# Kernel tuning notes

Measured on AMD Instinct MI355X. Metric: run time of the kernel, lower is better.

Reference implementation:

```python
import jax, jax.numpy as jnp
import numpy as np

N = 8192   # number of nodes / relationships
D = 64     # input_dim == output_dim


def setup_inputs() -> dict:
    key = jax.random.key(0)
    ks = jax.random.split(key, 13)
    s = 0.05
    return {
        "object_features": jax.random.normal(ks[0], (N, D), dtype=jnp.float32),
        "relationship_features": jax.random.normal(ks[1], (N, D), dtype=jnp.float32),
        # sparse-ish 0/1 adjacency, as in the reference usage
        "adjacency_matrix": (jax.random.uniform(ks[2], (N, N)) < 0.05).astype(jnp.float32),
        # nn.Linear params, stored as [in, out] (i.e. torch weight transposed)
        "W_obj": jax.random.normal(ks[3], (D, D), dtype=jnp.float32) * s,
        "b_obj": jax.random.normal(ks[4], (D,), dtype=jnp.float32) * s,
        "W_nobj": jax.random.normal(ks[5], (D, D), dtype=jnp.float32) * s,
        "b_nobj": jax.random.normal(ks[6], (D,), dtype=jnp.float32) * s,
        "W_rel": jax.random.normal(ks[7], (D, D), dtype=jnp.float32) * s,
        "b_rel": jax.random.normal(ks[8], (D,), dtype=jnp.float32) * s,
        "W_skip": jax.random.normal(ks[9], (D, D), dtype=jnp.float32) * s,
        "b_skip": jax.random.normal(ks[10], (D,), dtype=jnp.float32) * s,
        "Wa_w": jax.random.normal(ks[11], (2 * D, 1), dtype=jnp.float32) * s,  # Linear(2D -> 1)
        "Wa_b": jax.random.normal(ks[12], (1,), dtype=jnp.float32) * s,
    }


def reference(object_features, relationship_features, adjacency_matrix,
              W_obj, b_obj, W_nobj, b_nobj, W_rel, b_rel,
              W_skip, b_skip, Wa_w, Wa_b):
    x, r, A = object_features, relationship_features, adjacency_matrix
    d = x.shape[1]

    # message projections (small GEMMs)
    msgs_obj = x @ W_obj + b_obj                      # [N, D]
    msgs_nbr = A.T @ (x @ W_nobj + b_nobj)            # [N, D]
    msgs_rel = r @ W_rel + b_rel                      # [N, D]
    aggregated = msgs_obj + msgs_nbr + msgs_rel       # [N, D]

    # Wa(concat([x_i, r_j])) = x_i @ Wa_w[:d] + r_j @ Wa_w[d:] + Wa_b
    # (avoids materializing the [N, N, 2D] concat the torch code builds)
    sx = x @ Wa_w[:d]                                 # [N, 1] (per row i)
    sr = r @ Wa_w[d:]                                 # [N, 1] (per col j)
    scores = (sx + sr.T + Wa_b) * A                   # [N, N], masked-by-multiply
    attention = jax.nn.softmax(scores, axis=1)        # [N, N]

    # sum_j attn[i, j] * aggregated[i, :]  (exactly the torch broadcast-sum over dim=1)
    attn_agg = jnp.einsum('ij,ik->ik', attention, aggregated)  # [N, D]

    return x @ W_skip + b_skip + attn_agg
```

## Files before the change

kernel.cpp:

```cpp
#include <hip/hip_runtime.h>

typedef __attribute__((ext_vector_type(8))) short short8;
typedef __attribute__((ext_vector_type(4))) float f32x4;

#define NN 8192
#define DD 64

__device__ inline unsigned short f2bf(float f){
  unsigned b = __float_as_uint(f);
  b = (b + 0x7fffu + ((b >> 16) & 1u)) >> 16;
  return (unsigned short)b;
}


__global__ __launch_bounds__(256) void k_proj(
    const float* __restrict__ x, const float* __restrict__ r,
    const float* __restrict__ Wobj,  const float* __restrict__ bobj,
    const float* __restrict__ Wnobj, const float* __restrict__ bnobj,
    const float* __restrict__ Wrel,  const float* __restrict__ brel,
    const float* __restrict__ Wskip, const float* __restrict__ bskip,
    float* __restrict__ accT, unsigned short* __restrict__ yT)
{
  const int i  = blockIdx.x * 256 + threadIdx.x;
  const int d0 = blockIdx.y * 4;

  float ay[4] = {0.f,0.f,0.f,0.f}, az[4] = {0.f,0.f,0.f,0.f};
  const float4* xp = (const float4*)(x + (size_t)i * DD);
  const float4* rp = (const float4*)(r + (size_t)i * DD);

#pragma unroll
  for (int kb = 0; kb < 4; kb++){
    float xv[16], rv[16];
#pragma unroll
    for (int p = 0; p < 4; p++){
      float4 u = xp[kb*4 + p];
      xv[4*p+0]=u.x; xv[4*p+1]=u.y; xv[4*p+2]=u.z; xv[4*p+3]=u.w;
      float4 v = rp[kb*4 + p];
      rv[4*p+0]=v.x; rv[4*p+1]=v.y; rv[4*p+2]=v.z; rv[4*p+3]=v.w;
    }
#pragma unroll
    for (int kk = 0; kk < 16; kk++){
      const int wb = (kb*16 + kk) * DD + d0;
      const float xk = xv[kk], rk = rv[kk];
#pragma unroll
      for (int t = 0; t < 4; t++){
        ay[t] += xk * Wnobj[wb + t];
        az[t] += xk * Wobj [wb + t];
        az[t] += xk * Wskip[wb + t];
        az[t] += rk * Wrel [wb + t];
      }
    }
  }

#pragma unroll
  for (int t = 0; t < 4; t++){
    ay[t] += bnobj[d0 + t];
    az[t] += bobj[d0 + t] + brel[d0 + t] + bskip[d0 + t];
    yT[(size_t)(d0 + t) * NN + i]   = f2bf(ay[t]);
    accT[(size_t)(d0 + t) * NN + i] = az[t];
  }
}

#define BN 128
#define KSPLIT 8
#define KCH (NN / KSPLIT)
#define NIT (KCH / 64)
#define ASZ (64 * 128)
#define YSZ (64 * 72)

__global__ __launch_bounds__(256) void k_spmm(
    const float* __restrict__ A,
    const unsigned short* __restrict__ yT,
    float* __restrict__ part)
{
  __shared__ short Alds[2 * ASZ];
  __shared__ short Ylds[2 * YSZ];

  const int tid  = threadIdx.x;
  const int lane = tid & 63;
  const int wave = tid >> 6;
  const int q    = lane >> 4;
  const int nn   = lane & 15;

  const int j0     = blockIdx.x * BN;
  const int kstart = blockIdx.y * KCH;

  const int c4 = tid & 31;
  const int kr = tid >> 5;
  const int cY = tid & 7;
  const int m0 = tid >> 3;

  const float* ap          = A  + (size_t)(kstart + kr) * NN + j0 + c4 * 4;
  const unsigned short* yp = yT + (size_t)m0 * NN + kstart + cY * 8;

  uint4 abuf[8], ybuf[2];
  auto gload = [&](){
#pragma unroll
    for (int p = 0; p < 8; p++)
      abuf[p] = *(const uint4*)(ap + (size_t)p * 8 * NN);
#pragma unroll
    for (int p = 0; p < 2; p++)
      ybuf[p] = *(const uint4*)(yp + (size_t)p * 32 * NN);
    ap += 64 * NN;
    yp += 64;
  };
  auto stage = [&](int buf){
    short* Ab = &Alds[buf * ASZ];
    short* Yb = &Ylds[buf * YSZ];
#pragma unroll
    for (int p = 0; p < 8; p++){
      const int kk  = kr + p*8;
      const int key = 2 * (p & 3);
      unsigned lo = (abuf[p].y & 0xFFFF0000u) | (abuf[p].x >> 16);
      unsigned hi = (abuf[p].w & 0xFFFF0000u) | (abuf[p].z >> 16);
      *(uint2*)(&Ab[kk * 128 + (((c4 >> 1) ^ key) * 8) + (c4 & 1) * 4]) =
          make_uint2(lo, hi);
    }
#pragma unroll
    for (int p = 0; p < 2; p++)
      *(uint4*)(&Yb[(m0 + p*32) * 72 + cY * 8]) = ybuf[p];
  };

  f32x4 acc[4][2];
#pragma unroll
  for (int a = 0; a < 4; a++)
#pragma unroll
    for (int b = 0; b < 2; b++)
      acc[a][b] = (f32x4){0.f, 0.f, 0.f, 0.f};

  gload();
  stage(0);
  __syncthreads();

  for (int it = 0; it < NIT; ++it){
    if (it + 1 < NIT) gload();
    const short* Ab = &Alds[(it & 1) * ASZ];
    const short* Yb = &Ylds[(it & 1) * YSZ];

#pragma unroll
    for (int ks = 0; ks < 2; ks++){
      short8 af[4];
#pragma unroll
      for (int mt = 0; mt < 4; mt++)
        af[mt] = *(const short8*)(&Yb[(mt*16 + nn) * 72 + ks*32 + q*8]);
#pragma unroll
      for (int nt = 0; nt < 2; nt++){
        const int col = wave * 32 + nt * 16 + nn;
        const short* bp = &Ab[(ks*32 + q*8) * 128
                              + (((col >> 3) ^ (2*q)) * 8) + (col & 7)];
        short8 bf;
#pragma unroll
        for (int jj = 0; jj < 8; jj++) bf[jj] = bp[jj * 128];
#pragma unroll
        for (int mt = 0; mt < 4; mt++)
          acc[mt][nt] = __builtin_amdgcn_mfma_f32_16x16x32_bf16(af[mt], bf, acc[mt][nt], 0, 0, 0);
      }
    }

    if (it + 1 < NIT){
      stage((it + 1) & 1);
      __syncthreads();
    }
  }

  float* pp = part + (size_t)blockIdx.y * DD * NN;
#pragma unroll
  for (int mt = 0; mt < 4; mt++)
#pragma unroll
    for (int nt = 0; nt < 2; nt++)
#pragma unroll
      for (int v = 0; v < 4; v++){
        const int d   = mt * 16 + q * 4 + v;
        const int col = j0 + wave * 32 + nt * 16 + nn;
        pp[(size_t)d * NN + col] = acc[mt][nt][v];
      }
}

__global__ __launch_bounds__(256) void k_out(
    const float* __restrict__ accT, const float* __restrict__ part,
    float* __restrict__ out)
{
  __shared__ float t[64][33];
  const int tid = threadIdx.x;
  const int jb  = blockIdx.x * 32;

#pragma unroll
  for (int rep = 0; rep < 8; rep++){
    const int d = rep * 8 + (tid >> 5);
    const int j = tid & 31;
    const size_t base = (size_t)d * NN + jb + j;
    float s = accT[base];
#pragma unroll
    for (int kb = 0; kb < KSPLIT; kb++)
      s += part[(size_t)kb * DD * NN + base];
    t[d][j] = s;
  }
  __syncthreads();
#pragma unroll
  for (int rep = 0; rep < 8; rep++){
    const int j = rep * 4 + (tid >> 6);
    const int d = tid & 63;
    out[(size_t)(jb + j) * DD + d] = t[d][j];
  }
}

extern "C" void kernel_launch(void* const* d_in, const int* in_sizes, int n_in,
                              void* d_out, int out_size, void* d_ws, size_t ws_size,
                              hipStream_t stream) {
  const float* x     = (const float*)d_in[0];
  const float* r     = (const float*)d_in[1];
  const float* A     = (const float*)d_in[2];
  const float* Wobj  = (const float*)d_in[3];
  const float* bobj  = (const float*)d_in[4];
  const float* Wnobj = (const float*)d_in[5];
  const float* bnobj = (const float*)d_in[6];
  const float* Wrel  = (const float*)d_in[7];
  const float* brel  = (const float*)d_in[8];
  const float* Wskip = (const float*)d_in[9];
  const float* bskip = (const float*)d_in[10];

  char* ws = (char*)d_ws;
  float* accT        = (float*)ws;
  unsigned short* yT = (unsigned short*)(ws + (size_t)DD*NN*4);
  float* part        = (float*)(ws + 3u*1024*1024);

  k_proj<<<dim3(32, 16), 256, 0, stream>>>(x, r, Wobj, bobj, Wnobj, bnobj,
                                           Wrel, brel, Wskip, bskip, accT, yT);
  k_spmm<<<dim3(NN / BN, KSPLIT), 256, 0, stream>>>(A, yT, part);
  k_out<<<NN / 32, 256, 0, stream>>>(accT, part, (float*)d_out);
}
```

Baseline: 414.5 us.

## Widen SpMM column tile, halve K step, double K-split, use nontemporal loads

The SpMM kernel now uses 256-column block tiles with each wave covering 64 columns (four MFMA column tiles instead of two). The per-iteration K depth drops from 64 to 32 and the K-split grows from 8 to 16, so the grid stays at 512 blocks. Thread-to-load mappings and the LDS layouts for A and Y change to match. The streaming reads of A and of the partial sums in the reduction kernel become nontemporal loads to avoid polluting the cache. In exchange the partial-sum buffer doubles in size, which adds global writes and reads in the final reduction and needs more workspace.

```diff
diff --git a/kernel.cpp b/kernel.cpp
--- a/kernel.cpp
+++ b/kernel.cpp
@@ -2,6 +2,7 @@
 
 typedef __attribute__((ext_vector_type(8))) short short8;
 typedef __attribute__((ext_vector_type(4))) float f32x4;
+typedef __attribute__((ext_vector_type(4))) unsigned int u32x4;
 
 #define NN 8192
 #define DD 64
@@ -61,12 +62,14 @@
   }
 }
 
-#define BN 128
-#define KSPLIT 8
+#define BN 256
+#define KSPLIT 16
 #define KCH (NN / KSPLIT)
-#define NIT (KCH / 64)
-#define ASZ (64 * 128)
-#define YSZ (64 * 72)
+#define KT 32
+#define NIT (KCH / KT)
+#define ASZ (KT * BN)
+#define YPITCH 40
+#define YSZ (DD * YPITCH)
 
 __global__ __launch_bounds__(256) void k_spmm(
     const float* __restrict__ A,
@@ -85,47 +88,43 @@
   const int j0     = blockIdx.x * BN;
   const int kstart = blockIdx.y * KCH;
 
-  const int c4 = tid & 31;
-  const int kr = tid >> 5;
-  const int cY = tid & 7;
-  const int m0 = tid >> 3;
+  const int c4 = tid & 63;
+  const int kr = tid >> 6;
+  const int cY = tid & 3;
+  const int m  = tid >> 2;
 
   const float* ap          = A  + (size_t)(kstart + kr) * NN + j0 + c4 * 4;
-  const unsigned short* yp = yT + (size_t)m0 * NN + kstart + cY * 8;
-
-  uint4 abuf[8], ybuf[2];
+  const unsigned short* yp = yT + (size_t)m * NN + kstart + cY * 8;
+
+  u32x4 abuf[8]; uint4 ybuf;
   auto gload = [&](){
 #pragma unroll
     for (int p = 0; p < 8; p++)
-      abuf[p] = *(const uint4*)(ap + (size_t)p * 8 * NN);
-#pragma unroll
-    for (int p = 0; p < 2; p++)
-      ybuf[p] = *(const uint4*)(yp + (size_t)p * 32 * NN);
-    ap += 64 * NN;
-    yp += 64;
+      abuf[p] = __builtin_nontemporal_load((const u32x4*)(ap + (size_t)p * 4 * NN));
+    ybuf = *(const uint4*)yp;
+    ap += (size_t)KT * NN;
+    yp += KT;
   };
   auto stage = [&](int buf){
     short* Ab = &Alds[buf * ASZ];
     short* Yb = &Ylds[buf * YSZ];
 #pragma unroll
     for (int p = 0; p < 8; p++){
-      const int kk  = kr + p*8;
-      const int key = 2 * (p & 3);
-      unsigned lo = (abuf[p].y & 0xFFFF0000u) | (abuf[p].x >> 16);
-      unsigned hi = (abuf[p].w & 0xFFFF0000u) | (abuf[p].z >> 16);
-      *(uint2*)(&Ab[kk * 128 + (((c4 >> 1) ^ key) * 8) + (c4 & 1) * 4]) =
+      const int kk  = kr + p*4;
+      const int key = 2 * ((kk >> 3) & 3);
+      unsigned lo = (abuf[p][1] & 0xFFFF0000u) | (abuf[p][0] >> 16);
+      unsigned hi = (abuf[p][3] & 0xFFFF0000u) | (abuf[p][2] >> 16);
+      *(uint2*)(&Ab[kk * BN + (((c4 >> 1) ^ key) * 8) + (c4 & 1) * 4]) =
           make_uint2(lo, hi);
     }
-#pragma unroll
-    for (int p = 0; p < 2; p++)
-      *(uint4*)(&Yb[(m0 + p*32) * 72 + cY * 8]) = ybuf[p];
+    *(uint4*)(&Yb[m * YPITCH + cY * 8]) = ybuf;
   };
 
-  f32x4 acc[4][2];
+  f32x4 acc[4][4];
 #pragma unroll
   for (int a = 0; a < 4; a++)
 #pragma unroll
-    for (int b = 0; b < 2; b++)
+    for (int b = 0; b < 4; b++)
       acc[a][b] = (f32x4){0.f, 0.f, 0.f, 0.f};
 
   gload();
@@ -137,24 +136,20 @@
     const short* Ab = &Alds[(it & 1) * ASZ];
     const short* Yb = &Ylds[(it & 1) * YSZ];
 
-#pragma unroll
-    for (int ks = 0; ks < 2; ks++){
-      short8 af[4];
+    short8 af[4];
+#pragma unroll
+    for (int mt = 0; mt < 4; mt++)
+      af[mt] = *(const short8*)(&Yb[(mt*16 + nn) * YPITCH + q*8]);
+#pragma unroll
+    for (int nt = 0; nt < 4; nt++){
+      const int col = wave * 64 + nt * 16 + nn;
+      const short* bp = &Ab[(q*8) * BN + (((col >> 3) ^ (2*q)) * 8) + (col & 7)];
+      short8 bf;
+#pragma unroll
+      for (int jj = 0; jj < 8; jj++) bf[jj] = bp[jj * BN];
 #pragma unroll
       for (int mt = 0; mt < 4; mt++)
-        af[mt] = *(const short8*)(&Yb[(mt*16 + nn) * 72 + ks*32 + q*8]);
-#pragma unroll
-      for (int nt = 0; nt < 2; nt++){
-        const int col = wave * 32 + nt * 16 + nn;
-        const short* bp = &Ab[(ks*32 + q*8) * 128
-                              + (((col >> 3) ^ (2*q)) * 8) + (col & 7)];
-        short8 bf;
-#pragma unroll
-        for (int jj = 0; jj < 8; jj++) bf[jj] = bp[jj * 128];
-#pragma unroll
-        for (int mt = 0; mt < 4; mt++)
-          acc[mt][nt] = __builtin_amdgcn_mfma_f32_16x16x32_bf16(af[mt], bf, acc[mt][nt], 0, 0, 0);
-      }
+        acc[mt][nt] = __builtin_amdgcn_mfma_f32_16x16x32_bf16(af[mt], bf, acc[mt][nt], 0, 0, 0);
     }
 
     if (it + 1 < NIT){
@@ -167,11 +162,11 @@
 #pragma unroll
   for (int mt = 0; mt < 4; mt++)
 #pragma unroll
-    for (int nt = 0; nt < 2; nt++)
+    for (int nt = 0; nt < 4; nt++)
 #pragma unroll
       for (int v = 0; v < 4; v++){
         const int d   = mt * 16 + q * 4 + v;
-        const int col = j0 + wave * 32 + nt * 16 + nn;
+        const int col = j0 + wave * 64 + nt * 16 + nn;
         pp[(size_t)d * NN + col] = acc[mt][nt][v];
       }
 }
@@ -192,7 +187,7 @@
     float s = accT[base];
 #pragma unroll
     for (int kb = 0; kb < KSPLIT; kb++)
-      s += part[(size_t)kb * DD * NN + base];
+      s += __builtin_nontemporal_load(part + (size_t)kb * DD * NN + base);
     t[d][j] = s;
   }
   __syncthreads();
```

Result: no change. 408.3 us, median of 2 (-1.5%).
